# Kernel tuning notes

Measured on AMD Instinct MI355X. Metric: run time of the kernel, lower is better.

Reference implementation:

```python
import jax, jax.numpy as jnp
import numpy as np

N = 30000   # nodes
E = 600000  # edges
IN = 256    # in_channels
HID = 128   # 2*out_channels
OUT = 64    # out_channels


def setup_inputs() -> dict:
    key = jax.random.key(0)
    k = jax.random.split(key, 6)
    x = jax.random.normal(k[0], (N, IN), dtype=jnp.float32)
    edge_index = jax.random.randint(k[1], (2, E), 0, N, dtype=jnp.int64)
    W1 = jax.random.normal(k[2], (IN, HID), dtype=jnp.float32) * (1.0 / np.sqrt(IN))
    b1 = jnp.zeros((HID,), dtype=jnp.float32)
    W2 = jax.random.normal(k[3], (HID, OUT), dtype=jnp.float32) * (1.0 / np.sqrt(HID))
    b2 = jnp.zeros((OUT,), dtype=jnp.float32)
    return {"x": x, "edge_index": edge_index, "W1": W1, "b1": b1, "W2": W2, "b2": b2}


def _gcn_norm(edge_index, n_nodes):
    # PyG gcn_norm with add_self_loops=True, edge_weight=1
    loop = jnp.arange(n_nodes, dtype=edge_index.dtype)
    src = jnp.concatenate([edge_index[0], loop])
    dst = jnp.concatenate([edge_index[1], loop])
    deg = jax.ops.segment_sum(jnp.ones_like(dst, dtype=jnp.float32), dst,
                              num_segments=n_nodes)
    dinv = jnp.where(deg > 0, jax.lax.rsqrt(deg), 0.0)
    norm = dinv[src] * dinv[dst]  # [E+N]
    return src, dst, norm


def _gcn_conv(h, src, dst, norm, W, b, n_nodes):
    h = h @ W                              # [N, out] linear first (PyG order)
    msg = h[src] * norm[:, None]           # gather + per-edge scale, [E+N, out]
    out = jax.ops.segment_sum(msg, dst, num_segments=n_nodes)  # scatter-add
    return out + b


def reference(x, edge_index, W1, b1, W2, b2):
    n_nodes = x.shape[0]
    src, dst, norm = _gcn_norm(edge_index, n_nodes)
    h = _gcn_conv(x, src, dst, norm, W1, b1, n_nodes)
    h = jax.nn.relu(h)
    return _gcn_conv(h, src, dst, norm, W2, b2, n_nodes)
```

## Files before the change

### kernel.cpp

```cpp
#include <hip/hip_runtime.h>


#define GCN_IN 256
#define GCN_HID 128
#define GCN_OUT 64

#define BKT 128
#define SBE 4096
#define SRCM 0x1FFFFFFu

typedef unsigned short ushort_t;
typedef __attribute__((ext_vector_type(8))) short short8;
typedef __attribute__((ext_vector_type(8))) unsigned short ushort8;
typedef __attribute__((ext_vector_type(4))) float f32x4;

__device__ inline float bf2f(ushort_t u) {
  union { unsigned int i; float f; } x; x.i = ((unsigned int)u) << 16; return x.f;
}
__device__ inline ushort_t f2bf(float f) {
  union { float f; unsigned int i; } u; u.f = f;
  unsigned int r = u.i + 0x7FFFu + ((u.i >> 16) & 1u);
  return (ushort_t)(r >> 16);
}

__global__ void probe_kernel(const ushort_t* __restrict__ xu,
                             const int* __restrict__ ei,
                             int* __restrict__ flags) {
  int lane = threadIdx.x;
  int c = 0, nz = 0;
  for (int i = lane; i < 128; i += 64) {
    ushort_t u = xu[2 * i];
    int e = (u >> 7) & 0xFF;
    c += (e >= 100 && e <= 140) ? 1 : 0;
    nz += (ei[2 * i + 1] != 0) ? 1 : 0;
  }
  for (int off = 32; off > 0; off >>= 1) {
    c += __shfl_down(c, off);
    nz += __shfl_down(nz, off);
  }
  if (lane == 0) {
    flags[0] = (c >= 64) ? 0 : 1;
    flags[1] = (nz == 0) ? 1 : 0;
  }
}

__global__ void hist_kernel(const int* __restrict__ ei, int E,
                            int* __restrict__ Hmat, int nsb, int nbin,
                            const int* __restrict__ flags) {
  __shared__ int hist[256];
  int t = threadIdx.x;
  int sb = blockIdx.x;
  hist[t] = 0;
  __syncthreads();
  int base = sb * SBE;
  int end = base + SBE; if (end > E) end = E;
  bool i64 = flags[1] != 0;
  for (int i = base + t; i < end; i += 256) {
    int d = i64 ? ei[2 * E + 2 * i] : ei[E + i];
    atomicAdd(&hist[d >> 7], 1);
  }
  __syncthreads();
  for (int b = t; b < nbin; b += 256)
    Hmat[b * nsb + sb] = hist[b];
}

__global__ void scanA_kernel(const int* __restrict__ Hmat, int nsb,
                             int* __restrict__ binsum) {
  __shared__ int red[256];
  int t = threadIdx.x;
  const int* row = Hmat + (size_t)blockIdx.x * nsb;
  int s = 0;
  for (int i = t; i < nsb; i += 256) s += row[i];
  red[t] = s;
  __syncthreads();
  for (int off = 128; off > 0; off >>= 1) {
    if (t < off) red[t] += red[t + off];
    __syncthreads();
  }
  if (t == 0) binsum[blockIdx.x] = red[0];
}

__global__ void scanB_kernel(int* __restrict__ binsum, int nbin) {
  __shared__ int red[256];
  int t = threadIdx.x;
  int self = (t < nbin) ? binsum[t] : 0;
  red[t] = self;
  __syncthreads();
  for (int off = 1; off < 256; off <<= 1) {
    int u = (t >= off) ? red[t - off] : 0;
    __syncthreads();
    red[t] += u;
    __syncthreads();
  }
  if (t < nbin) binsum[t] = red[t] - self;
}

__global__ void scanC_kernel(int* __restrict__ Hmat, int nsb,
                             const int* __restrict__ binsum) {
  __shared__ int red[256];
  int t = threadIdx.x;
  int* row = Hmat + (size_t)blockIdx.x * nsb;
  int self = (t < nsb) ? row[t] : 0;
  red[t] = self;
  __syncthreads();
  for (int off = 1; off < 256; off <<= 1) {
    int u = (t >= off) ? red[t - off] : 0;
    __syncthreads();
    red[t] += u;
    __syncthreads();
  }
  if (t < nsb) row[t] = binsum[blockIdx.x] + red[t] - self;
}

__global__ void stage2_kernel(const int* __restrict__ ei, int E,
                              const int* __restrict__ Hscan, int nsb, int nbin,
                              unsigned int* __restrict__ stage,
                              const int* __restrict__ flags) {
  __shared__ int cur[256];
  int t = threadIdx.x;
  int sb = blockIdx.x;
  for (int b = t; b < nbin; b += 256)
    cur[b] = Hscan[b * nsb + sb];
  __syncthreads();
  int base = sb * SBE;
  int end = base + SBE; if (end > E) end = E;
  bool i64 = flags[1] != 0;
  for (int i = base + t; i < end; i += 256) {
    int s, d;
    if (i64) { s = ei[2 * i]; d = ei[2 * E + 2 * i]; }
    else     { s = ei[i];     d = ei[E + i]; }
    int pos = atomicAdd(&cur[d >> 7], 1);
    stage[pos] = (unsigned int)s | ((unsigned int)(d & 127) << 25);
  }
}

__global__ void scatter_kernel(const unsigned int* __restrict__ stage,
                               const int* __restrict__ Hmat, int nsb, int nbin,
                               int* __restrict__ csr_src,
                               int* __restrict__ row_ptr,
                               float* __restrict__ dinv, int n, int E) {
  __shared__ int lcnt[BKT];
  __shared__ int lscan[BKT];
  __shared__ int lcur[BKT];
  const int t = threadIdx.x;
  const int b = blockIdx.x;
  const int node0 = b * BKT;
  const int nn = (n - node0 < BKT) ? (n - node0) : BKT;
  const int rb = Hmat[b * nsb];
  const int re = (b + 1 < nbin) ? Hmat[(b + 1) * nsb] : E;
  if (t < BKT) lcnt[t] = 0;
  __syncthreads();
  for (int i = rb + t; i < re; i += 256)
    atomicAdd(&lcnt[stage[i] >> 25], 1);
  __syncthreads();
  if (t < BKT) lscan[t] = lcnt[t];
  __syncthreads();
  for (int off = 1; off < BKT; off <<= 1) {
    int v = 0;
    if (t < BKT && t >= off) v = lscan[t - off];
    __syncthreads();
    if (t < BKT) lscan[t] += v;
    __syncthreads();
  }
  if (t < BKT) {
    int excl = rb + lscan[t] - lcnt[t];
    lcur[t] = excl;
    if (t < nn) {
      row_ptr[node0 + t] = excl;
      dinv[node0 + t] = rsqrtf((float)(lcnt[t] + 1));
    }
  }
  if (t == 0 && node0 + nn == n) row_ptr[n] = E;
  __syncthreads();
  for (int i = rb + t; i < re; i += 256) {
    unsigned int p = stage[i];
    int l = p >> 25;
    int pos = atomicAdd(&lcur[l], 1);
    csr_src[pos] = (int)(p & SRCM);
  }
}

__global__ void prep_w_kernel(const void* __restrict__ W1, const void* __restrict__ W2,
                              ushort_t* __restrict__ Wt1, ushort_t* __restrict__ Wt2,
                              const int* __restrict__ flags) {
  int i = blockIdx.x * blockDim.x + threadIdx.x;
  bool f32 = flags[0] != 0;
  if (i < GCN_IN * GCN_HID) {
    int k = i >> 7, n = i & 127;
    float v = f32 ? ((const float*)W1)[i] : bf2f(((const ushort_t*)W1)[i]);
    Wt1[n * GCN_IN + k] = f2bf(v);
  }
  int j = i - GCN_IN * GCN_HID;
  if (j >= 0 && j < GCN_HID * GCN_OUT) {
    int k = j >> 6, n = j & 63;
    float v = f32 ? ((const float*)W2)[j] : bf2f(((const ushort_t*)W2)[j]);
    Wt2[n * GCN_HID + k] = f2bf(v);
  }
}

template<int K, int NC, int A_MODE>
__global__ __launch_bounds__(256)
void gemm_mfma_kernel(const void* __restrict__ A, const ushort_t* __restrict__ Bt,
                      ushort_t* __restrict__ C, int M, const int* __restrict__ flags) {
  constexpr int KT = 32;
  constexpr int NT = NC / 32;
  __shared__ ushort_t As[32 * KT];
  __shared__ ushort_t Bs[NC * KT];
  const int tid = threadIdx.x;
  const int wv = tid >> 6;
  const int lane = tid & 63;
  const int ml = lane & 15;
  const int quad = lane >> 4;
  const int row0 = blockIdx.x * 32;
  const int mrow = (wv & 1) * 16 + ml;
  const int ncol0 = (wv >> 1) * (NC / 2);
  const bool aF32 = (A_MODE == 0) && (flags[0] != 0);
  f32x4 acc[NT] = {};

  for (int kt = 0; kt < K; kt += KT) {
    for (int c = tid; c < 32 * KT / 8; c += 256) {
      int r = c >> 2, cq = c & 3;
      ushort8 o;
      if (row0 + r < M) {
        if (aF32) {
          const float* ap = (const float*)A + (size_t)(row0 + r) * K + kt + cq * 8;
          float4 f0 = *(const float4*)ap;
          float4 f1 = *(const float4*)(ap + 4);
          o[0] = f2bf(f0.x); o[1] = f2bf(f0.y); o[2] = f2bf(f0.z); o[3] = f2bf(f0.w);
          o[4] = f2bf(f1.x); o[5] = f2bf(f1.y); o[6] = f2bf(f1.z); o[7] = f2bf(f1.w);
        } else {
          o = *(const ushort8*)((const ushort_t*)A + (size_t)(row0 + r) * K + kt + cq * 8);
        }
      } else {
        o = (ushort8)0;
      }
      *(ushort8*)&As[c * 8] = o;
    }
    for (int c = tid; c < NC * KT / 8; c += 256) {
      int n = c >> 2, cq = c & 3;
      *(ushort8*)&Bs[c * 8] = *(const ushort8*)(Bt + (size_t)n * K + kt + cq * 8);
    }
    __syncthreads();
    short8 af = *(const short8*)&As[mrow * KT + quad * 8];
#pragma unroll
    for (int t = 0; t < NT; ++t) {
      short8 bf = *(const short8*)&Bs[(ncol0 + t * 16 + ml) * KT + quad * 8];
      acc[t] = __builtin_amdgcn_mfma_f32_16x16x32_bf16(af, bf, acc[t], 0, 0, 0);
    }
    __syncthreads();
  }

  const int orow = row0 + (wv & 1) * 16 + quad * 4;
#pragma unroll
  for (int t = 0; t < NT; ++t) {
    int col = ncol0 + t * 16 + ml;
#pragma unroll
    for (int r = 0; r < 4; ++r) {
      if (orow + r < M)
        C[(size_t)(orow + r) * NC + col] = f2bf(acc[t][r]);
    }
  }
}


__global__ void aggregate_relu_kernel(const ushort_t* __restrict__ h,
                                      const int* __restrict__ row_ptr,
                                      const int* __restrict__ csr_src,
                                      const float* __restrict__ dinv,
                                      const void* __restrict__ bias,
                                      ushort_t* __restrict__ outp, int n,
                                      const int* __restrict__ flags) {
  int wave = threadIdx.x >> 6;
  int lane = threadIdx.x & 63;
  int v = blockIdx.x * (blockDim.x >> 6) + wave;
  if (v >= n) return;
  const int q = lane & 15, g = lane >> 4;
  float acc[8] = {};
  int beg = row_ptr[v], end = row_ptr[v + 1];
  for (int base = beg; base < end; base += 64) {
    int navail = end - base; if (navail > 64) navail = 64;
    int sv = 0; float dv = 0.f;
    if (base + lane < end) { sv = csr_src[base + lane]; dv = dinv[sv]; }
    for (int j = 0; j < navail; j += 4) {
      int e = j + g;
      int s = __shfl(sv, e);
      float ds = __shfl(dv, e);
      ushort8 hv = *(const ushort8*)(h + (size_t)s * GCN_HID + q * 8);
#pragma unroll
      for (int k = 0; k < 8; ++k) acc[k] = fmaf(ds, bf2f(hv[k]), acc[k]);
    }
  }
#pragma unroll
  for (int k = 0; k < 8; ++k) {
    acc[k] += __shfl_xor(acc[k], 16);
    acc[k] += __shfl_xor(acc[k], 32);
  }
  if (g == 0) {
    float di = dinv[v];
    float sl = di * di;
    ushort8 hv = *(const ushort8*)(h + (size_t)v * GCN_HID + q * 8);
    const bool bF32 = flags[0] != 0;
    ushort8 o;
#pragma unroll
    for (int k = 0; k < 8; ++k) {
      float bv = bF32 ? ((const float*)bias)[q * 8 + k]
                      : bf2f(((const ushort_t*)bias)[q * 8 + k]);
      o[k] = f2bf(fmaxf(di * acc[k] + sl * bf2f(hv[k]) + bv, 0.f));
    }
    *(ushort8*)(outp + (size_t)v * GCN_HID + q * 8) = o;
  }
}

__global__ void aggregate_out_kernel(const ushort_t* __restrict__ h,
                                     const int* __restrict__ row_ptr,
                                     const int* __restrict__ csr_src,
                                     const float* __restrict__ dinv,
                                     const void* __restrict__ bias,
                                     void* __restrict__ outp, int n,
                                     const int* __restrict__ flags) {
  int wave = threadIdx.x >> 6;
  int lane = threadIdx.x & 63;
  int v = blockIdx.x * (blockDim.x >> 6) + wave;
  if (v >= n) return;
  const int q = lane & 7, g = lane >> 3;
  float acc[8] = {};
  int beg = row_ptr[v], end = row_ptr[v + 1];
  for (int base = beg; base < end; base += 64) {
    int navail = end - base; if (navail > 64) navail = 64;
    int sv = 0; float dv = 0.f;
    if (base + lane < end) { sv = csr_src[base + lane]; dv = dinv[sv]; }
    for (int j = 0; j < navail; j += 8) {
      int e = j + g;
      int s = __shfl(sv, e);
      float ds = __shfl(dv, e);
      ushort8 hv = *(const ushort8*)(h + (size_t)s * GCN_OUT + q * 8);
#pragma unroll
      for (int k = 0; k < 8; ++k) acc[k] = fmaf(ds, bf2f(hv[k]), acc[k]);
    }
  }
#pragma unroll
  for (int k = 0; k < 8; ++k) {
    acc[k] += __shfl_xor(acc[k], 8);
    acc[k] += __shfl_xor(acc[k], 16);
    acc[k] += __shfl_xor(acc[k], 32);
  }
  if (g == 0) {
    float di = dinv[v];
    float sl = di * di;
    ushort8 hv = *(const ushort8*)(h + (size_t)v * GCN_OUT + q * 8);
    const bool oF32 = flags[0] != 0;
    float r[8];
#pragma unroll
    for (int k = 0; k < 8; ++k) {
      float bv = oF32 ? ((const float*)bias)[q * 8 + k]
                      : bf2f(((const ushort_t*)bias)[q * 8 + k]);
      r[k] = di * acc[k] + sl * bf2f(hv[k]) + bv;
    }
    if (oF32) {
      float* op = (float*)outp + (size_t)v * GCN_OUT + q * 8;
      *(float4*)op = make_float4(r[0], r[1], r[2], r[3]);
      *(float4*)(op + 4) = make_float4(r[4], r[5], r[6], r[7]);
    } else {
      ushort8 o;
#pragma unroll
      for (int k = 0; k < 8; ++k) o[k] = f2bf(r[k]);
      *(ushort8*)((ushort_t*)outp + (size_t)v * GCN_OUT + q * 8) = o;
    }
  }
}


extern "C" void kernel_launch(void* const* d_in, const int* in_sizes, int n_in,
                              void* d_out, int out_size, void* d_ws, size_t ws_size,
                              hipStream_t stream) {
  const void* x  = d_in[0];
  const int*  ei = (const int*)d_in[1];
  const void* W1 = d_in[2];
  const void* b1 = d_in[3];
  const void* W2 = d_in[4];
  const void* b2 = d_in[5];

  const int N = in_sizes[0] / GCN_IN;
  const int E = in_sizes[1] / 2;
  const int nsb  = (E + SBE - 1) / SBE;
  const int nbin = (N + BKT - 1) / BKT;

  size_t off = 0;
  auto alloc = [&](size_t bytes) -> void* {
    void* p = (char*)d_ws + off;
    off += (bytes + 255) & ~(size_t)255;
    return p;
  };
  int*          flags   = (int*)alloc(256);
  int*          binsum  = (int*)alloc(256 * 4);
  int*          Hmat    = (int*)alloc((size_t)nbin * nsb * 4);
  unsigned int* stage   = (unsigned int*)alloc((size_t)E * 4);
  int*          csr_src = (int*)alloc((size_t)E * 4);
  int*          row_ptr = (int*)alloc((size_t)(N + 1) * 4);
  float*        dinv    = (float*)alloc((size_t)N * 4);
  ushort_t*     h1      = (ushort_t*)alloc((size_t)N * GCN_HID * 2);
  ushort_t*     hag     = (ushort_t*)alloc((size_t)N * GCN_HID * 2);
  ushort_t*     wt1     = (ushort_t*)alloc((size_t)GCN_HID * GCN_IN * 2);
  ushort_t*     wt2     = (ushort_t*)alloc((size_t)GCN_OUT * GCN_HID * 2);
  ushort_t*     h2      = h1;

  probe_kernel<<<1, 64, 0, stream>>>((const ushort_t*)x, ei, flags);
  hist_kernel<<<nsb, 256, 0, stream>>>(ei, E, Hmat, nsb, nbin, flags);
  scanA_kernel<<<nbin, 256, 0, stream>>>(Hmat, nsb, binsum);
  scanB_kernel<<<1, 256, 0, stream>>>(binsum, nbin);
  scanC_kernel<<<nbin, 256, 0, stream>>>(Hmat, nsb, binsum);
  stage2_kernel<<<nsb, 256, 0, stream>>>(ei, E, Hmat, nsb, nbin, stage, flags);
  scatter_kernel<<<nbin, 256, 0, stream>>>(stage, Hmat, nsb, nbin, csr_src,
                                           row_ptr, dinv, N, E);

  prep_w_kernel<<<(GCN_IN * GCN_HID + GCN_HID * GCN_OUT + 255) / 256, 256, 0, stream>>>(
      W1, W2, wt1, wt2, flags);

  gemm_mfma_kernel<GCN_IN, GCN_HID, 0>
      <<<(N + 31) / 32, 256, 0, stream>>>(x, wt1, h1, N, flags);

  int gAgg = (N + 3) / 4;
  aggregate_relu_kernel<<<gAgg, 256, 0, stream>>>(h1, row_ptr, csr_src,
                                                  dinv, b1, hag, N, flags);

  gemm_mfma_kernel<GCN_HID, GCN_OUT, 2>
      <<<(N + 31) / 32, 256, 0, stream>>>(hag, wt2, h2, N, flags);

  aggregate_out_kernel<<<gAgg, 256, 0, stream>>>(h2, row_ptr, csr_src,
                                                 dinv, b2, d_out, N, flags);
}
```

Before: 176.3 us.

## Fuse layer-2 linear into layer-1 aggregation and merge scan kernels

The layer-1 aggregation kernel now applies bias and ReLU and then multiplies each node's 128-wide row by W2 inside the same wave, using shuffles and per-lane W2 rows. This drops the hag intermediate write and read and removes the second MFMA GEMM launch. The scanB kernel is folded into scanC, with each block redundantly recomputing the bin-sum prefix, which saves one launch. The fused matvec runs on scalar FMAs with 128 shuffles per node instead of MFMA, so per-node ALU work in the aggregation rises.

```diff
diff --git a/kernel.cpp b/kernel.cpp
--- a/kernel.cpp
+++ b/kernel.cpp
@@ -80,25 +80,24 @@
   if (t == 0) binsum[blockIdx.x] = red[0];
 }
 
-__global__ void scanB_kernel(int* __restrict__ binsum, int nbin) {
+__global__ void scanC_kernel(int* __restrict__ Hmat, int nsb,
+                             const int* __restrict__ binsum, int nbin) {
+  __shared__ int bred[256];
   __shared__ int red[256];
   int t = threadIdx.x;
-  int self = (t < nbin) ? binsum[t] : 0;
-  red[t] = self;
+  int bs = (t < nbin) ? binsum[t] : 0;
+  bred[t] = bs;
   __syncthreads();
   for (int off = 1; off < 256; off <<= 1) {
-    int u = (t >= off) ? red[t - off] : 0;
-    __syncthreads();
-    red[t] += u;
-    __syncthreads();
-  }
-  if (t < nbin) binsum[t] = red[t] - self;
-}
-
-__global__ void scanC_kernel(int* __restrict__ Hmat, int nsb,
-                             const int* __restrict__ binsum) {
-  __shared__ int red[256];
-  int t = threadIdx.x;
+    int u = (t >= off) ? bred[t - off] : 0;
+    __syncthreads();
+    bred[t] += u;
+    __syncthreads();
+  }
+  __shared__ int seed_sh;
+  if (t == (int)blockIdx.x) seed_sh = bred[t] - bs;
+  __syncthreads();
+  int seed = seed_sh;
   int* row = Hmat + (size_t)blockIdx.x * nsb;
   int self = (t < nsb) ? row[t] : 0;
   red[t] = self;
@@ -109,7 +108,7 @@
     red[t] += u;
     __syncthreads();
   }
-  if (t < nsb) row[t] = binsum[blockIdx.x] + red[t] - self;
+  if (t < nsb) row[t] = seed + red[t] - self;
 }
 
 __global__ void stage2_kernel(const int* __restrict__ ei, int E,
@@ -263,13 +262,14 @@
 }
 
 
-__global__ void aggregate_relu_kernel(const ushort_t* __restrict__ h,
-                                      const int* __restrict__ row_ptr,
-                                      const int* __restrict__ csr_src,
-                                      const float* __restrict__ dinv,
-                                      const void* __restrict__ bias,
-                                      ushort_t* __restrict__ outp, int n,
-                                      const int* __restrict__ flags) {
+__global__ void agg1_fused_kernel(const ushort_t* __restrict__ h,
+                                  const int* __restrict__ row_ptr,
+                                  const int* __restrict__ csr_src,
+                                  const float* __restrict__ dinv,
+                                  const void* __restrict__ bias,
+                                  const ushort_t* __restrict__ wt2,
+                                  ushort_t* __restrict__ h2out,
+                                  int n, const int* __restrict__ flags) {
   int wave = threadIdx.x >> 6;
   int lane = threadIdx.x & 63;
   int v = blockIdx.x * (blockDim.x >> 6) + wave;
@@ -295,20 +295,27 @@
     acc[k] += __shfl_xor(acc[k], 16);
     acc[k] += __shfl_xor(acc[k], 32);
   }
-  if (g == 0) {
-    float di = dinv[v];
-    float sl = di * di;
-    ushort8 hv = *(const ushort8*)(h + (size_t)v * GCN_HID + q * 8);
-    const bool bF32 = flags[0] != 0;
-    ushort8 o;
-#pragma unroll
-    for (int k = 0; k < 8; ++k) {
-      float bv = bF32 ? ((const float*)bias)[q * 8 + k]
-                      : bf2f(((const ushort_t*)bias)[q * 8 + k]);
-      o[k] = f2bf(fmaxf(di * acc[k] + sl * bf2f(hv[k]) + bv, 0.f));
-    }
-    *(ushort8*)(outp + (size_t)v * GCN_HID + q * 8) = o;
-  }
+  float di = dinv[v];
+  float sl = di * di;
+  ushort8 hv = *(const ushort8*)(h + (size_t)v * GCN_HID + q * 8);
+  const bool bF32 = flags[0] != 0;
+  float hagv[8];
+#pragma unroll
+  for (int k = 0; k < 8; ++k) {
+    float bv = bF32 ? ((const float*)bias)[q * 8 + k]
+                    : bf2f(((const ushort_t*)bias)[q * 8 + k]);
+    hagv[k] = fmaxf(di * acc[k] + sl * bf2f(hv[k]) + bv, 0.f);
+  }
+  float h2a = 0.f;
+  const ushort_t* wrow = wt2 + (size_t)lane * GCN_HID;
+#pragma unroll
+  for (int kq = 0; kq < 16; ++kq) {
+    ushort8 w = *(const ushort8*)(wrow + kq * 8);
+#pragma unroll
+    for (int j = 0; j < 8; ++j)
+      h2a = fmaf(__shfl(hagv[j], kq), bf2f(w[j]), h2a);
+  }
+  h2out[(size_t)v * GCN_OUT + lane] = f2bf(h2a);
 }
 
 __global__ void aggregate_out_kernel(const ushort_t* __restrict__ h,
@@ -399,16 +406,14 @@
   int*          row_ptr = (int*)alloc((size_t)(N + 1) * 4);
   float*        dinv    = (float*)alloc((size_t)N * 4);
   ushort_t*     h1      = (ushort_t*)alloc((size_t)N * GCN_HID * 2);
-  ushort_t*     hag     = (ushort_t*)alloc((size_t)N * GCN_HID * 2);
+  ushort_t*     h2      = (ushort_t*)alloc((size_t)N * GCN_OUT * 2);
   ushort_t*     wt1     = (ushort_t*)alloc((size_t)GCN_HID * GCN_IN * 2);
   ushort_t*     wt2     = (ushort_t*)alloc((size_t)GCN_OUT * GCN_HID * 2);
-  ushort_t*     h2      = h1;
 
   probe_kernel<<<1, 64, 0, stream>>>((const ushort_t*)x, ei, flags);
   hist_kernel<<<nsb, 256, 0, stream>>>(ei, E, Hmat, nsb, nbin, flags);
   scanA_kernel<<<nbin, 256, 0, stream>>>(Hmat, nsb, binsum);
-  scanB_kernel<<<1, 256, 0, stream>>>(binsum, nbin);
-  scanC_kernel<<<nbin, 256, 0, stream>>>(Hmat, nsb, binsum);
+  scanC_kernel<<<nbin, 256, 0, stream>>>(Hmat, nsb, binsum, nbin);
   stage2_kernel<<<nsb, 256, 0, stream>>>(ei, E, Hmat, nsb, nbin, stage, flags);
   scatter_kernel<<<nbin, 256, 0, stream>>>(stage, Hmat, nsb, nbin, csr_src,
                                            row_ptr, dinv, N, E);
@@ -420,11 +425,8 @@
       <<<(N + 31) / 32, 256, 0, stream>>>(x, wt1, h1, N, flags);
 
   int gAgg = (N + 3) / 4;
-  aggregate_relu_kernel<<<gAgg, 256, 0, stream>>>(h1, row_ptr, csr_src,
-                                                  dinv, b1, hag, N, flags);
-
-  gemm_mfma_kernel<GCN_HID, GCN_OUT, 2>
-      <<<(N + 31) / 32, 256, 0, stream>>>(hag, wt2, h2, N, flags);
+  agg1_fused_kernel<<<gAgg, 256, 0, stream>>>(h1, row_ptr, csr_src, dinv, b1,
+                                              wt2, h2, N, flags);
 
   aggregate_out_kernel<<<gAgg, 256, 0, stream>>>(h2, row_ptr, csr_src,
                                                  dinv, b2, d_out, N, flags);
```

Result: slower. 237.1 us (+34.5%).
